# Kernel tuning notes

Measured on AMD Instinct MI355X. Metric: run time of the kernel, lower is better.

## Reference

```python
import jax, jax.numpy as jnp
import numpy as np
from jax import lax

G = 8      # deform groups (weight groups == offset groups)
K = 3      # kernel size
K2 = K * K


def conv3x3(x, w, b):
    # NCHW, 3x3, stride 1, padding 1 (SAME)
    y = lax.conv_general_dilated(x, w, (1, 1), 'SAME',
                                 dimension_numbers=('NCHW', 'OIHW', 'NCHW'))
    return y + b[None, :, None, None]


def deform_conv2d(ref, offsets, w, b):
    # ref: [B,C,H,W], offsets: [B,2*G*K2,H,W] (torchvision layout: per group,
    # per kernel position, (dy, dx) pairs), w: [C_out, C_in/G, K, K], b: [C_out]
    B, C, H, W = ref.shape
    Cg = C // G
    off = offsets.reshape(B, G, K2, 2, H, W)
    dy = off[:, :, :, 0]  # [B,G,K2,H,W]
    dx = off[:, :, :, 1]
    ky = (jnp.arange(K2) // K - K // 2).astype(ref.dtype)  # kernel y offsets (pad=1)
    kx = (jnp.arange(K2) % K - K // 2).astype(ref.dtype)
    base_y = jnp.arange(H, dtype=ref.dtype)[:, None] + ky[:, None, None]  # [K2,H,1]
    base_x = jnp.arange(W, dtype=ref.dtype)[None, :] + kx[:, None, None]  # [K2,1,W]
    py = dy + base_y  # [B,G,K2,H,W]
    px = dx + base_x

    y0 = jnp.floor(py).astype(jnp.int32)
    x0 = jnp.floor(px).astype(jnp.int32)
    ly = py - y0.astype(ref.dtype)
    lx = px - x0.astype(ref.dtype)

    ref_flat = ref.reshape(B, G, Cg, H * W)

    def gather(yi, xi):
        valid = (yi >= 0) & (yi < H) & (xi >= 0) & (xi < W)
        idx = jnp.clip(yi, 0, H - 1) * W + jnp.clip(xi, 0, W - 1)  # [B,G,K2,H,W]
        vals = jnp.take_along_axis(ref_flat, idx.reshape(B, G, 1, K2 * H * W), axis=3)
        vals = vals.reshape(B, G, Cg, K2, H, W)
        return vals * valid[:, :, None].astype(ref.dtype)

    w00 = ((1 - ly) * (1 - lx))[:, :, None]
    w01 = ((1 - ly) * lx)[:, :, None]
    w10 = (ly * (1 - lx))[:, :, None]
    w11 = (ly * lx)[:, :, None]
    sampled = (w00 * gather(y0, x0) + w01 * gather(y0, x0 + 1)
               + w10 * gather(y0 + 1, x0) + w11 * gather(y0 + 1, x0 + 1))
    # grouped accumulation: weight [C_out, Cg, K, K] -> [G, OCg, Cg, K2]
    wg = w.reshape(G, C // G, Cg, K2)
    out = jnp.einsum('bgikhw,goik->bgohw', sampled, wg)
    return out.reshape(B, C, H, W) + b[None, :, None, None]


def setup_inputs() -> dict:
    key = jax.random.key(0)
    ks = jax.random.split(key, 10)
    B, C, H, W = 2, 64, 256, 256
    s64 = 1.0 / np.sqrt(C * 9)
    s128 = 1.0 / np.sqrt(128 * 9)
    return {
        'offset': jax.random.normal(ks[0], (B, C, H, W), jnp.float32),
        'ref': jax.random.normal(ks[1], (B, C, H, W), jnp.float32),
        'w_off': jax.random.normal(ks[2], (2 * K2 * G, C, K, K), jnp.float32) * s64,
        'b_off': jnp.zeros((2 * K2 * G,), jnp.float32),
        'w_def': jax.random.normal(ks[3], (C, C // G, K, K), jnp.float32) * (1.0 / np.sqrt((C // G) * 9)),
        'b_def': jnp.zeros((C,), jnp.float32),
        'w_r1': jax.random.normal(ks[4], (C, 2 * C, K, K), jnp.float32) * s128,
        'b_r1': jnp.zeros((C,), jnp.float32),
        'w_r2': jax.random.normal(ks[5], (C, C, K, K), jnp.float32) * s64,
        'b_r2': jnp.zeros((C,), jnp.float32),
    }


def reference(offset, ref, w_off, b_off, w_def, b_def, w_r1, b_r1, w_r2, b_r2):
    deform_offsets = conv3x3(offset, w_off, b_off)              # [B,144,H,W]
    aligned_ref = deform_conv2d(ref, deform_offsets, w_def, b_def)
    x = jnp.concatenate([ref, aligned_ref], axis=1)             # [B,128,H,W]
    x = jax.nn.relu(conv3x3(x, w_r1, b_r1))
    x = jax.nn.relu(conv3x3(x, w_r2, b_r2))
    return x + aligned_ref
```

## Files before the change

kernel.cpp:

```cpp
#include <hip/hip_runtime.h>

typedef __attribute__((ext_vector_type(8)))  short  short8;
typedef __attribute__((ext_vector_type(4)))  float  float4v;
typedef __attribute__((ext_vector_type(16))) float  float16v;

constexpr int HH = 256, WW = 256;
constexpr int PD = 258;
constexpr size_t HWsz = (size_t)HH * WW;

__device__ inline unsigned short f2bf(float f) {
    unsigned int u = __builtin_bit_cast(unsigned int, f);
    u += 0x7FFFu + ((u >> 16) & 1u);
    return (unsigned short)(u >> 16);
}
__device__ inline float bfhalf(unsigned int w, int hi) {
    return __builtin_bit_cast(float, hi ? (w & 0xFFFF0000u) : (w << 16));
}

template<int CDST, bool WRITE_G>
__global__ __launch_bounds__(256) void nchw_to_nhwc(
    const float* __restrict__ src, unsigned short* __restrict__ dst,
    unsigned short* __restrict__ dst_g)
{
    const int px = threadIdx.x, h = blockIdx.x, bi = blockIdx.y;
    const float* s = src + (size_t)bi * 64 * HWsz + (size_t)h * WW + px;
    unsigned short* d = dst + (((size_t)bi * PD + (h + 1)) * PD + (px + 1)) * CDST;
#pragma unroll
    for (int cg = 0; cg < 8; ++cg) {
        float v[8];
#pragma unroll
        for (int j = 0; j < 8; ++j) v[j] = s[(size_t)(cg * 8 + j) * HWsz];
        uint4 pk;
        pk.x = f2bf(v[0]) | ((unsigned)f2bf(v[1]) << 16);
        pk.y = f2bf(v[2]) | ((unsigned)f2bf(v[3]) << 16);
        pk.z = f2bf(v[4]) | ((unsigned)f2bf(v[5]) << 16);
        pk.w = f2bf(v[6]) | ((unsigned)f2bf(v[7]) << 16);
        *(uint4*)&d[cg * 8] = pk;
        if (WRITE_G) {
            unsigned short* dg = dst_g +
                (((size_t)(bi * 8 + cg) * HWsz) + (size_t)h * WW + px) * 8;
            *(uint4*)dg = pk;
        }
    }
}

__global__ __launch_bounds__(256) void zero_border(
    unsigned short* __restrict__ p_off, unsigned short* __restrict__ p_cat,
    unsigned short* __restrict__ p_x1)
{
    const int bi = blockIdx.y, which = blockIdx.z;
    unsigned short* buf = which == 0 ? p_off : (which == 1 ? p_cat : p_x1);
    const int CIN = (which == 1) ? 128 : 64;
    const int NG = CIN / 8;
    unsigned short* p = buf + (size_t)bi * PD * PD * CIN;
    const int total = 1028 * 16;
    for (int i = blockIdx.x * 256 + threadIdx.x; i < total; i += gridDim.x * 256) {
        int g = i & 15;
        if (g >= NG) continue;
        int pxi = i >> 4;
        int r, c;
        if (pxi < 258)       { r = 0;   c = pxi; }
        else if (pxi < 516)  { r = 257; c = pxi - 258; }
        else if (pxi < 772)  { r = pxi - 516 + 1; c = 0; }
        else                 { r = pxi - 772 + 1; c = 257; }
        uint4 z = {0, 0, 0, 0};
        *(uint4*)&p[((size_t)r * PD + c) * CIN + g * 8] = z;
    }
}

__device__ inline void pack_one(const float* __restrict__ w, short* __restrict__ wpk,
                                int Cout, int Cin, int e)
{
    int j = e & 7;
    int lane = (e >> 3) & 63;
    int ksp = 9 * (Cin / 16);
    int kstep = (e >> 9) % ksp;
    int cot = (e >> 9) / ksp;
    int tap = kstep / (Cin / 16);
    int ci = (kstep % (Cin / 16)) * 16 + (lane >> 5) * 8 + j;
    int co = cot * 32 + (lane & 31);
    float v = (co < Cout) ? w[((size_t)co * Cin + ci) * 9 + tap] : 0.f;
    wpk[e] = (short)f2bf(v);
}

__global__ __launch_bounds__(256) void pack_all(
    const float* __restrict__ w1, short* __restrict__ d1,
    const float* __restrict__ w2, short* __restrict__ d2,
    const float* __restrict__ w3, short* __restrict__ d3)
{
    int e = blockIdx.x * 256 + threadIdx.x;
    if (e < 110592)               pack_one(w1, d1, 144, 64, e);
    else if (e < 110592 + 73728)  pack_one(w2, d2, 64, 128, e - 110592);
    else if (e < 221184)          pack_one(w3, d3, 64, 64,  e - 184320);
}

template<int CIN, int MODE, int COTB>
__global__ __launch_bounds__(256, 2) void conv_mfma32(
    const unsigned short* __restrict__ src,
    const short* __restrict__ wpk,
    const float* __restrict__ bias,
    unsigned short* __restrict__ dst_bf,
    float* __restrict__ dst_f,
    const unsigned short* __restrict__ resid_bf)
{
    constexpr int CHUNKS = CIN / 32;
    constexpr int KST = 9 * (CIN / 16);

    __shared__ unsigned short lds[3 * 258 * 32];

    const int tid  = threadIdx.x;
    const int lane = tid & 63;
    const int wv   = tid >> 6;
    const int half = lane >> 5;
    const int n32  = lane & 31;
    const int h  = blockIdx.x;
    const int bi = blockIdx.y / COTB;
    const int cb = blockIdx.y % COTB;

    const unsigned short* srcB = src + (size_t)bi * PD * PD * CIN;
    const short8* wbase = (const short8*)wpk;

    float16v acc[2][2];
#pragma unroll
    for (int coF = 0; coF < 2; ++coF) {
        float16v bv;
#pragma unroll
        for (int reg = 0; reg < 16; ++reg) {
            int co = cb * 64 + coF * 32 + (reg >> 2) * 8 + 4 * half + (reg & 3);
            float b = 0.f;
            if (MODE != 0 || co < 144) b = bias[co];
            bv[reg] = b;
        }
        acc[coF][0] = bv;
        acc[coF][1] = bv;
    }

    for (int ch = 0; ch < CHUNKS; ++ch) {
        __syncthreads();
#pragma unroll
        for (int r = 0; r < 3; ++r) {
            const unsigned short* grow = srcB + ((size_t)(h + r) * PD) * CIN + ch * 32;
            for (int q = tid; q < 1032; q += 256) {
                int pc = q >> 2, g = q & 3;
                uint4 v = *(const uint4*)(grow + (size_t)pc * CIN + g * 8);
                int gsw = g ^ ((pc >> 1) & 3);
                *(uint4*)&lds[((size_t)r * 258 + pc) * 32 + gsw * 8] = v;
            }
        }
        __syncthreads();

#pragma unroll
        for (int tap = 0; tap < 9; ++tap) {
            const int row = tap / 3, dxo = tap % 3;
#pragma unroll
            for (int s = 0; s < 2; ++s) {
                const int kstep = tap * (CIN / 16) + ch * 2 + s;
                short8 a0 = wbase[((size_t)(cb * 2 + 0) * KST + kstep) * 64 + lane];
                short8 a1 = wbase[((size_t)(cb * 2 + 1) * KST + kstep) * 64 + lane];
#pragma unroll
                for (int nt = 0; nt < 2; ++nt) {
                    int pc = wv * 64 + nt * 32 + n32 + dxo;
                    int gsw = (s * 2 + half) ^ ((pc >> 1) & 3);
                    short8 b = *(const short8*)&lds[((size_t)row * 258 + pc) * 32 + gsw * 8];
                    acc[0][nt] = __builtin_amdgcn_mfma_f32_32x32x16_bf16(a0, b, acc[0][nt], 0, 0, 0);
                    acc[1][nt] = __builtin_amdgcn_mfma_f32_32x32x16_bf16(a1, b, acc[1][nt], 0, 0, 0);
                }
            }
        }
    }

#pragma unroll
    for (int coF = 0; coF < 2; ++coF) {
#pragma unroll
        for (int nt = 0; nt < 2; ++nt) {
            const int px = wv * 64 + nt * 32 + n32;
            float16v a = acc[coF][nt];
#pragma unroll
            for (int q = 0; q < 4; ++q) {
                const int co4 = cb * 64 + coF * 32 + q * 8 + 4 * half;
                float v0 = a[q * 4 + 0], v1 = a[q * 4 + 1];
                float v2 = a[q * 4 + 2], v3 = a[q * 4 + 3];
                if (MODE == 0) {
                    if (co4 < 144) {
                        unsigned short* d = dst_bf + (size_t)bi * HWsz * 144;
                        uint2 pk;
                        pk.x = f2bf(v0) | ((unsigned)f2bf(v1) << 16);
                        pk.y = f2bf(v2) | ((unsigned)f2bf(v3) << 16);
                        *(uint2*)&d[((size_t)h * WW + px) * 144 + co4] = pk;
                    }
                } else if (MODE == 1) {
                    unsigned short* d = dst_bf + (size_t)bi * PD * PD * 64;
                    uint2 pk;
                    pk.x = f2bf(fmaxf(v0, 0.f)) | ((unsigned)f2bf(fmaxf(v1, 0.f)) << 16);
                    pk.y = f2bf(fmaxf(v2, 0.f)) | ((unsigned)f2bf(fmaxf(v3, 0.f)) << 16);
                    *(uint2*)&d[(((size_t)h + 1) * PD + (px + 1)) * 64 + co4] = pk;
                } else {
                    const unsigned short* rp = resid_bf + (size_t)bi * PD * PD * 128;
                    uint2 rv = *(const uint2*)&rp[(((size_t)h + 1) * PD + (px + 1)) * 128 + 64 + co4];
                    float r0 = bfhalf(rv.x, 0), r1 = bfhalf(rv.x, 1);
                    float r2 = bfhalf(rv.y, 0), r3 = bfhalf(rv.y, 1);
                    float* d = dst_f + (size_t)bi * 64 * HWsz + (size_t)h * WW + px;
                    d[(size_t)(co4 + 0) * HWsz] = fmaxf(v0, 0.f) + r0;
                    d[(size_t)(co4 + 1) * HWsz] = fmaxf(v1, 0.f) + r1;
                    d[(size_t)(co4 + 2) * HWsz] = fmaxf(v2, 0.f) + r2;
                    d[(size_t)(co4 + 3) * HWsz] = fmaxf(v3, 0.f) + r3;
                }
            }
        }
    }
}

__global__ __launch_bounds__(256) void deform_k5(
    const unsigned short* __restrict__ refg,
    const unsigned short* __restrict__ doff,
    const float* __restrict__ wdef, const float* __restrict__ bdef,
    unsigned short* __restrict__ pcat_out)
{
    __shared__ float wsm2[576];
    const int L = blockIdx.x;
    const int xcd = L & 7;
    const int j = L >> 3;
    const int g = j & 7;
    const int r = (j >> 3) & 31;
    const int bi = j >> 8;
    const int h = xcd * 32 + r;
    const int px = threadIdx.x;

    for (int i = threadIdx.x; i < 576; i += 256) {
        int o = i & 7, c = (i >> 3) & 7, k = i >> 6;
        wsm2[i] = wdef[(size_t)g * 576 + o * 72 + c * 9 + k];
    }
    __syncthreads();

    const unsigned int* dp = (const unsigned int*)(
        doff + (((size_t)bi * HWsz) + (size_t)h * WW + px) * 144 + g * 18);
    unsigned int dw[9];
#pragma unroll
    for (int k = 0; k < 9; ++k) dw[k] = dp[k];

    float acc[8];
#pragma unroll
    for (int o = 0; o < 8; ++o) acc[o] = bdef[g * 8 + o];

    const unsigned short* rb = refg + (size_t)(bi * 8 + g) * HWsz * 8;

#pragma unroll
    for (int k = 0; k < 9; ++k) {
        float dy = bfhalf(dw[k], 0);
        float dx = bfhalf(dw[k], 1);
        float py = dy + (float)(h + k / 3 - 1);
        float pxs = dx + (float)(px + k % 3 - 1);
        float fy = floorf(py), fx = floorf(pxs);
        int y0 = (int)fy, x0i = (int)fx;
        float ly = py - fy, lx = pxs - fx;
        int y1 = y0 + 1, x1i = x0i + 1;
        bool vy0 = (y0 >= 0) & (y0 < HH), vy1 = (y1 >= 0) & (y1 < HH);
        bool vx0 = (x0i >= 0) & (x0i < WW), vx1 = (x1i >= 0) & (x1i < WW);
        int cy0 = min(max(y0, 0), HH - 1), cy1 = min(max(y1, 0), HH - 1);
        int cx0 = min(max(x0i, 0), WW - 1), cx1 = min(max(x1i, 0), WW - 1);
        float w00 = (1.f - ly) * (1.f - lx), w01 = (1.f - ly) * lx;
        float w10 = ly * (1.f - lx), w11 = ly * lx;
        if (!(vy0 && vx0)) w00 = 0.f;
        if (!(vy0 && vx1)) w01 = 0.f;
        if (!(vy1 && vx0)) w10 = 0.f;
        if (!(vy1 && vx1)) w11 = 0.f;

        uint4 q00 = *(const uint4*)(rb + ((size_t)cy0 * WW + cx0) * 8);
        uint4 q01 = *(const uint4*)(rb + ((size_t)cy0 * WW + cx1) * 8);
        uint4 q10 = *(const uint4*)(rb + ((size_t)cy1 * WW + cx0) * 8);
        uint4 q11 = *(const uint4*)(rb + ((size_t)cy1 * WW + cx1) * 8);
        union U { uint4 v; unsigned int a[4]; };
        U u00{q00}, u01{q01}, u10{q10}, u11{q11};

#pragma unroll
        for (int cw = 0; cw < 4; ++cw) {
#pragma unroll
            for (int hl = 0; hl < 2; ++hl) {
                int c = cw * 2 + hl;
                float sv = w00 * bfhalf(u00.a[cw], hl) + w01 * bfhalf(u01.a[cw], hl)
                         + w10 * bfhalf(u10.a[cw], hl) + w11 * bfhalf(u11.a[cw], hl);
                const float* wp = &wsm2[((k * 8) + c) * 8];
                float4v wlo = *(const float4v*)wp;
                float4v whi = *(const float4v*)(wp + 4);
                acc[0] += wlo[0] * sv; acc[1] += wlo[1] * sv;
                acc[2] += wlo[2] * sv; acc[3] += wlo[3] * sv;
                acc[4] += whi[0] * sv; acc[5] += whi[1] * sv;
                acc[6] += whi[2] * sv; acc[7] += whi[3] * sv;
            }
        }
    }

    unsigned short* po = pcat_out + (((size_t)bi * PD + (h + 1)) * PD + (px + 1)) * 128 + 64 + g * 8;
    uint4 pk;
    pk.x = f2bf(acc[0]) | ((unsigned)f2bf(acc[1]) << 16);
    pk.y = f2bf(acc[2]) | ((unsigned)f2bf(acc[3]) << 16);
    pk.z = f2bf(acc[4]) | ((unsigned)f2bf(acc[5]) << 16);
    pk.w = f2bf(acc[6]) | ((unsigned)f2bf(acc[7]) << 16);
    *(uint4*)po = pk;
}

extern "C" void kernel_launch(void* const* d_in, const int* in_sizes, int n_in,
                              void* d_out, int out_size, void* d_ws, size_t ws_size,
                              hipStream_t stream)
{
    const float* offset = (const float*)d_in[0];
    const float* ref    = (const float*)d_in[1];
    const float* w_off  = (const float*)d_in[2];
    const float* b_off  = (const float*)d_in[3];
    const float* w_def  = (const float*)d_in[4];
    const float* b_def  = (const float*)d_in[5];
    const float* w_r1   = (const float*)d_in[6];
    const float* b_r1   = (const float*)d_in[7];
    const float* w_r2   = (const float*)d_in[8];
    const float* b_r2   = (const float*)d_in[9];
    float* out = (float*)d_out;

    unsigned short* p_off = (unsigned short*)d_ws;
    unsigned short* p_cat = p_off + (size_t)8520192;
    unsigned short* p_x1  = p_cat + (size_t)17040384;
    unsigned short* doff  = p_x1 + (size_t)8520192;
    unsigned short* refg  = doff + (size_t)18874368;
    short* wpk1  = (short*)(refg + (size_t)8388608);
    short* wpkr1 = wpk1 + 110592;
    short* wpkr2 = wpkr1 + 73728;

    zero_border<<<dim3(65, 2, 3), 256, 0, stream>>>(p_off, p_cat, p_x1);

    pack_all<<<dim3((221184 + 255) / 256), 256, 0, stream>>>(
        w_off, wpk1, w_r1, wpkr1, w_r2, wpkr2);

    nchw_to_nhwc<64, false><<<dim3(256, 2), 256, 0, stream>>>(offset, p_off, nullptr);
    nchw_to_nhwc<128, true><<<dim3(256, 2), 256, 0, stream>>>(ref, p_cat, refg);

    conv_mfma32<64, 0, 3><<<dim3(256, 6), 256, 0, stream>>>(
        p_off, wpk1, b_off, doff, nullptr, nullptr);

    deform_k5<<<dim3(4096), 256, 0, stream>>>(refg, doff, w_def, b_def, p_cat);

    conv_mfma32<128, 1, 1><<<dim3(256, 2), 256, 0, stream>>>(
        p_cat, wpkr1, b_r1, p_x1, nullptr, nullptr);

    conv_mfma32<64, 2, 1><<<dim3(256, 2), 256, 0, stream>>>(
        p_x1, wpkr2, b_r2, nullptr, out, p_cat);
}
```

Measured before the change: 342.9 us.

## Give each wave a private LDS slice to drop block barriers in conv

The 3x3 MFMA conv kernel now gives each wavefront its own LDS segment covering its 64-pixel band plus halo, loaded with a new padded layout instead of the XOR swizzle, so both __syncthreads per channel chunk are removed. The output-channel fragment count per block is now a template parameter, so the offset conv covers 96 channels per block over 4 grid slices instead of 64 over 6. Occupancy hints also rise to 3 blocks for the residual convs. The cost is duplicated halo loads per wave, more accumulator registers for the offset conv, and a different LDS bank pattern.

```diff
diff --git a/kernel.cpp b/kernel.cpp
--- a/kernel.cpp
+++ b/kernel.cpp
@@ -94,8 +94,8 @@
     else if (e < 221184)          pack_one(w3, d3, 64, 64,  e - 184320);
 }
 
-template<int CIN, int MODE, int COTB>
-__global__ __launch_bounds__(256, 2) void conv_mfma32(
+template<int CIN, int COF, int COTB, int MODE, int MINW>
+__global__ __launch_bounds__(256, MINW) void conv_mfma_nb(
     const unsigned short* __restrict__ src,
     const short* __restrict__ wpk,
     const float* __restrict__ bias,
@@ -105,8 +105,9 @@
 {
     constexpr int CHUNKS = CIN / 32;
     constexpr int KST = 9 * (CIN / 16);
-
-    __shared__ unsigned short lds[3 * 258 * 32];
+    constexpr int WSEG = 3 * 4 * 66 * 8;
+
+    __shared__ unsigned short lds[4 * WSEG];
 
     const int tid  = threadIdx.x;
     const int lane = tid & 63;
@@ -116,38 +117,40 @@
     const int h  = blockIdx.x;
     const int bi = blockIdx.y / COTB;
     const int cb = blockIdx.y % COTB;
-
+    const int cbase = cb * COF * 32;
+
+    unsigned short* my = lds + wv * WSEG;
     const unsigned short* srcB = src + (size_t)bi * PD * PD * CIN;
     const short8* wbase = (const short8*)wpk;
 
-    float16v acc[2][2];
-#pragma unroll
-    for (int coF = 0; coF < 2; ++coF) {
+    float16v acc[COF][2];
+#pragma unroll
+    for (int f = 0; f < COF; ++f) {
         float16v bv;
 #pragma unroll
         for (int reg = 0; reg < 16; ++reg) {
-            int co = cb * 64 + coF * 32 + (reg >> 2) * 8 + 4 * half + (reg & 3);
+            int co = cbase + f * 32 + (reg >> 2) * 8 + 4 * half + (reg & 3);
             float b = 0.f;
             if (MODE != 0 || co < 144) b = bias[co];
             bv[reg] = b;
         }
-        acc[coF][0] = bv;
-        acc[coF][1] = bv;
+        acc[f][0] = bv;
+        acc[f][1] = bv;
     }
 
     for (int ch = 0; ch < CHUNKS; ++ch) {
-        __syncthreads();
-#pragma unroll
-        for (int r = 0; r < 3; ++r) {
-            const unsigned short* grow = srcB + ((size_t)(h + r) * PD) * CIN + ch * 32;
-            for (int q = tid; q < 1032; q += 256) {
-                int pc = q >> 2, g = q & 3;
-                uint4 v = *(const uint4*)(grow + (size_t)pc * CIN + g * 8);
-                int gsw = g ^ ((pc >> 1) & 3);
-                *(uint4*)&lds[((size_t)r * 258 + pc) * 32 + gsw * 8] = v;
+        const unsigned short* gband = srcB + ((size_t)h * PD + wv * 64) * CIN + ch * 32;
+#pragma unroll
+        for (int i0 = 0; i0 < 264; i0 += 64) {
+            int i = i0 + lane;
+            if (i0 + 64 > 264 && i >= 264) continue;
+            int px = i >> 2, o = i & 3;
+#pragma unroll
+            for (int r = 0; r < 3; ++r) {
+                uint4 v = *(const uint4*)(gband + ((size_t)r * PD + px) * CIN + o * 8);
+                *(uint4*)&my[(((size_t)r * 4 + o) * 66 + px) * 8] = v;
             }
         }
-        __syncthreads();
 
 #pragma unroll
         for (int tap = 0; tap < 9; ++tap) {
@@ -155,29 +158,31 @@
 #pragma unroll
             for (int s = 0; s < 2; ++s) {
                 const int kstep = tap * (CIN / 16) + ch * 2 + s;
-                short8 a0 = wbase[((size_t)(cb * 2 + 0) * KST + kstep) * 64 + lane];
-                short8 a1 = wbase[((size_t)(cb * 2 + 1) * KST + kstep) * 64 + lane];
+                short8 a[COF];
+#pragma unroll
+                for (int f = 0; f < COF; ++f)
+                    a[f] = wbase[((size_t)(cb * COF + f) * KST + kstep) * 64 + lane];
 #pragma unroll
                 for (int nt = 0; nt < 2; ++nt) {
-                    int pc = wv * 64 + nt * 32 + n32 + dxo;
-                    int gsw = (s * 2 + half) ^ ((pc >> 1) & 3);
-                    short8 b = *(const short8*)&lds[((size_t)row * 258 + pc) * 32 + gsw * 8];
-                    acc[0][nt] = __builtin_amdgcn_mfma_f32_32x32x16_bf16(a0, b, acc[0][nt], 0, 0, 0);
-                    acc[1][nt] = __builtin_amdgcn_mfma_f32_32x32x16_bf16(a1, b, acc[1][nt], 0, 0, 0);
+                    short8 b = *(const short8*)
+                        &my[(((size_t)row * 4 + s * 2 + half) * 66 + nt * 32 + dxo + n32) * 8];
+#pragma unroll
+                    for (int f = 0; f < COF; ++f)
+                        acc[f][nt] = __builtin_amdgcn_mfma_f32_32x32x16_bf16(a[f], b, acc[f][nt], 0, 0, 0);
                 }
             }
         }
     }
 
 #pragma unroll
-    for (int coF = 0; coF < 2; ++coF) {
+    for (int f = 0; f < COF; ++f) {
 #pragma unroll
         for (int nt = 0; nt < 2; ++nt) {
             const int px = wv * 64 + nt * 32 + n32;
-            float16v a = acc[coF][nt];
+            float16v a = acc[f][nt];
 #pragma unroll
             for (int q = 0; q < 4; ++q) {
-                const int co4 = cb * 64 + coF * 32 + q * 8 + 4 * half;
+                const int co4 = cbase + f * 32 + q * 8 + 4 * half;
                 float v0 = a[q * 4 + 0], v1 = a[q * 4 + 1];
                 float v2 = a[q * 4 + 2], v3 = a[q * 4 + 3];
                 if (MODE == 0) {
@@ -332,14 +337,14 @@
     nchw_to_nhwc<64, false><<<dim3(256, 2), 256, 0, stream>>>(offset, p_off, nullptr);
     nchw_to_nhwc<128, true><<<dim3(256, 2), 256, 0, stream>>>(ref, p_cat, refg);
 
-    conv_mfma32<64, 0, 3><<<dim3(256, 6), 256, 0, stream>>>(
+    conv_mfma_nb<64, 3, 2, 0, 2><<<dim3(256, 4), 256, 0, stream>>>(
         p_off, wpk1, b_off, doff, nullptr, nullptr);
 
     deform_k5<<<dim3(4096), 256, 0, stream>>>(refg, doff, w_def, b_def, p_cat);
 
-    conv_mfma32<128, 1, 1><<<dim3(256, 2), 256, 0, stream>>>(
+    conv_mfma_nb<128, 2, 1, 1, 3><<<dim3(256, 2), 256, 0, stream>>>(
         p_cat, wpkr1, b_r1, p_x1, nullptr, nullptr);
 
-    conv_mfma32<64, 2, 1><<<dim3(256, 2), 256, 0, stream>>>(
+    conv_mfma_nb<64, 2, 1, 2, 3><<<dim3(256, 2), 256, 0, stream>>>(
         p_x1, wpkr2, b_r2, nullptr, out, p_cat);
 }
```

New measurement: 348.9 us. Within noise of the previous version (+1.7%).
